# Optimization experiments

Hardware: AMD Instinct MI355X
Metric: run time of the kernel (lower is better)

The kernel has to match this reference:

```python
import math
import jax, jax.numpy as jnp
import numpy as np

N_IMAGES = 32
TOTAL_Q = 2048
TOTAL_KV = 2048
Q_IN = 1024
KV_IN = Q_IN + 9
D_QK = 1024
D_V = 1024
N_HEADS = 16
TEMP = 1.0
SCALER = 1.0 / (TEMP * math.sqrt(D_QK // N_HEADS))


def _ragged_seg_ids(total, n_seg, seed):
    rng = np.random.default_rng(seed)
    lens = rng.multinomial(total - n_seg, np.ones(n_seg) / n_seg) + 1  # every segment nonempty
    return jnp.asarray(np.repeat(np.arange(n_seg), lens), dtype=jnp.int32)


def setup_inputs() -> dict:
    key = jax.random.key(0)
    ks = jax.random.split(key, 12)
    s = 0.02
    return {
        "A": jax.random.normal(ks[0], (TOTAL_Q, Q_IN), jnp.float32),
        "B0": jax.random.normal(ks[1], (TOTAL_KV, KV_IN), jnp.float32),
        "seg_q": _ragged_seg_ids(TOTAL_Q, N_IMAGES, 1),
        "seg_kv": _ragged_seg_ids(TOTAL_KV, N_IMAGES, 2),
        "Wq": jax.random.normal(ks[2], (Q_IN, D_QK), jnp.float32) * s,
        "bq": jax.random.normal(ks[3], (D_QK,), jnp.float32) * s,
        "Wk": jax.random.normal(ks[4], (KV_IN, D_QK), jnp.float32) * s,
        "bk": jax.random.normal(ks[5], (D_QK,), jnp.float32) * s,
        "Wv": jax.random.normal(ks[6], (KV_IN, D_V), jnp.float32) * s,
        "bv": jax.random.normal(ks[7], (D_V,), jnp.float32) * s,
        "Wf": jax.random.normal(ks[8], (D_V, Q_IN), jnp.float32) * s,
        "bf": jax.random.normal(ks[9], (Q_IN,), jnp.float32) * s,
    }


def reference(A, B0, seg_q, seg_kv, Wq, bq, Wk, bk, Wv, bv, Wf, bf):
    # Linear projections on packed rows
    q = (A @ Wq + bq).reshape(TOTAL_Q, N_HEADS, -1)     # [Nq, h, dqk]
    k = (B0 @ Wk + bk).reshape(TOTAL_KV, N_HEADS, -1)   # [Nk, h, dqk]
    v = (B0 @ Wv + bv).reshape(TOTAL_KV, N_HEADS, -1)   # [Nk, h, dv]
    # Per-segment attention expressed as a block mask (same math as the
    # original Python loop over splits)
    scores = jnp.einsum('ihd,khd->ihk', q, k) * SCALER  # [Nq, h, Nk]
    mask = (seg_q[:, None] == seg_kv[None, :])[:, None, :]  # [Nq, 1, Nk]
    neg = jnp.finfo(scores.dtype).min
    w = jax.nn.softmax(jnp.where(mask, scores, neg), axis=-1)
    wv = jnp.einsum('ihk,khd->ihd', w, v).reshape(TOTAL_Q, -1)  # [Nq, h*dv]
    return wv @ Wf + bf  # [Nq, q_in_dim]
```

## Files before the change

### kernel.cpp

```cpp
#include <hip/hip_runtime.h>
#include <hip/hip_bf16.h>
#include <math.h>

#define TOTAL_Q   2048
#define TOTAL_KV  2048
#define QIN       1024
#define KVIN      1033
#define KVIN_P    1056
#define DQK       1024
#define DV        1024
#define KVSTR     2048
#define SCALER    0.125f

typedef __bf16 bf16x8 __attribute__((ext_vector_type(8)));
typedef float  f32x4  __attribute__((ext_vector_type(4)));

__device__ __forceinline__ void glds16(const __hip_bfloat16* g, __bf16* l)
{
    __builtin_amdgcn_global_load_lds(
        (const __attribute__((address_space(1))) void*)g,
        (__attribute__((address_space(3))) void*)l,
        16, 0, 0);
}

__device__ __forceinline__ int stage_cc(int lane)
{
    return (((lane & 3) ^ ((lane >> 3) & 3)) * 8);
}
__device__ __forceinline__ int frag_off(int row, int quad)
{
    return row * 32 + ((quad ^ ((row >> 1) & 3)) * 8);
}

__global__ __launch_bounds__(256)
void prep_k(const float* __restrict__ A,  const float* __restrict__ B0,
            const float* __restrict__ Wq, const float* __restrict__ Wk,
            const float* __restrict__ Wv, const float* __restrict__ Wf,
            __hip_bfloat16* __restrict__ Abf, __hip_bfloat16* __restrict__ B0bf,
            __hip_bfloat16* __restrict__ Wqt, __hip_bfloat16* __restrict__ Wkt,
            __hip_bfloat16* __restrict__ Wvt, __hip_bfloat16* __restrict__ Wft)
{
    const int b   = blockIdx.x;
    const int tid = threadIdx.x;

    if (b < 2048) {
        int i = (b * 256 + tid) * 4;
        float4 f = *(const float4*)(A + i);
        __hip_bfloat16 o[4] = { __float2bfloat16(f.x), __float2bfloat16(f.y),
                                __float2bfloat16(f.z), __float2bfloat16(f.w) };
        *(uint2*)(Abf + i) = *(const uint2*)o;
        return;
    }
    if (b < 4160) {
        int idx = ((b - 2048) * 256 + tid) * 4;
        int r = idx / KVIN_P, c = idx - r * KVIN_P;
        __hip_bfloat16 o[4];
        #pragma unroll
        for (int j = 0; j < 4; ++j)
            o[j] = __float2bfloat16((c + j < KVIN) ? B0[(size_t)r * KVIN + c + j] : 0.f);
        *(uint2*)(B0bf + idx) = *(const uint2*)o;
        return;
    }

    const float* W; __hip_bfloat16* Wt; int K, Kp, k0, n0;
    if (b < 6208) {
        int z = b - 4160;
        W  = (z >= 1024) ? Wf : Wq;
        Wt = (z >= 1024) ? Wft : Wqt;
        K = 1024; Kp = 1024;
        int rem = z & 1023;
        k0 = (rem & 31) * 32; n0 = (rem >> 5) * 32;
    } else {
        int z = b - 6208;
        W  = (z >= 1056) ? Wv : Wk;
        Wt = (z >= 1056) ? Wvt : Wkt;
        K = KVIN; Kp = KVIN_P;
        int rem = (z >= 1056) ? z - 1056 : z;
        k0 = (rem % 33) * 32; n0 = (rem / 33) * 32;
    }
    const int tx = tid & 31, ty = tid >> 5;
    __shared__ float tile[32][33];
    #pragma unroll
    for (int i = 0; i < 4; ++i) {
        int k = k0 + ty + i * 8;
        tile[ty + i * 8][tx] = (k < K) ? W[(size_t)k * 1024 + n0 + tx] : 0.f;
    }
    __syncthreads();
    #pragma unroll
    for (int i = 0; i < 4; ++i) {
        int n = n0 + ty + i * 8;
        Wt[(size_t)n * Kp + k0 + tx] = __float2bfloat16(tile[tx][ty + i * 8]);
    }
}

__global__ __launch_bounds__(256)
void gemm_qkv(const __hip_bfloat16* __restrict__ Abf,
              const __hip_bfloat16* __restrict__ Wqt,
              const float* __restrict__ bq,
              __hip_bfloat16* __restrict__ qb,
              const __hip_bfloat16* __restrict__ B0bf,
              const __hip_bfloat16* __restrict__ Wkvt,
              const float* __restrict__ bk, const float* __restrict__ bv,
              __hip_bfloat16* __restrict__ kvb)
{
    __shared__ __bf16 As[128 * 32];
    __shared__ __bf16 Bs[64 * 32];

    int b = blockIdx.x;
    const __hip_bfloat16 *Ag, *Btg; const float *bias0, *bias1;
    __hip_bfloat16* C; int N, K, bx, by;
    if (b < 256) {
        Ag = Abf; Btg = Wqt; bias0 = bq; bias1 = bq; C = qb;
        N = 1024; K = 1024;
        int xcd = b & 7, i = b >> 3;
        int px = xcd & 3, py = xcd >> 2;
        bx = px * 4 + (i & 3);
        by = py * 8 + (i >> 2);
    } else {
        b -= 256;
        Ag = B0bf; Btg = Wkvt; bias0 = bk; bias1 = bv; C = kvb;
        N = 2048; K = KVIN_P;
        int xcd = b & 7, i = b >> 3;
        int px = xcd & 3, py = xcd >> 2;
        bx = px * 8 + (i & 7);
        by = py * 8 + (i >> 3);
    }
    const int row0 = by * 128, col0 = bx * 64;

    const int tid  = threadIdx.x;
    const int wave = tid >> 6, lane = tid & 63;
    const int quad = lane >> 4, l16 = lane & 15;
    const int wm = (wave >> 1) * 64, wn = (wave & 1) * 32;

    const int cr = lane >> 2;
    const int cc = stage_cc(lane);

    const __hip_bfloat16* gsrc[3];
    __bf16* ldst[3];
    #pragma unroll
    for (int i = 0; i < 3; ++i) {
        int c = wave * 3 + i;
        if (c < 8) {
            gsrc[i] = Ag  + (size_t)(row0 + c * 16 + cr) * K + cc;
            ldst[i] = &As[c * 512];
        } else {
            gsrc[i] = Btg + (size_t)(col0 + (c - 8) * 16 + cr) * K + cc;
            ldst[i] = &Bs[(c - 8) * 512];
        }
    }

    f32x4 acc[4][2] = {};

    for (int k0 = 0; k0 < K; k0 += 32) {
        #pragma unroll
        for (int i = 0; i < 3; ++i)
            glds16(gsrc[i] + k0, ldst[i]);
        __syncthreads();

        bf16x8 af[4], bfr[2];
        #pragma unroll
        for (int mi = 0; mi < 4; ++mi)
            af[mi] = *(const bf16x8*)&As[frag_off(wm + mi * 16 + l16, quad)];
        #pragma unroll
        for (int ni = 0; ni < 2; ++ni)
            bfr[ni] = *(const bf16x8*)&Bs[frag_off(wn + ni * 16 + l16, quad)];

        #pragma unroll
        for (int mi = 0; mi < 4; ++mi)
            #pragma unroll
            for (int ni = 0; ni < 2; ++ni)
                acc[mi][ni] = __builtin_amdgcn_mfma_f32_16x16x32_bf16(
                    af[mi], bfr[ni], acc[mi][ni], 0, 0, 0);
        __syncthreads();
    }

    #pragma unroll
    for (int mi = 0; mi < 4; ++mi) {
        #pragma unroll
        for (int ni = 0; ni < 2; ++ni) {
            const int col = col0 + wn + ni * 16 + l16;
            const float bia = (col < 1024) ? bias0[col] : bias1[col - 1024];
            #pragma unroll
            for (int r = 0; r < 4; ++r) {
                const int row = row0 + wm + mi * 16 + quad * 4 + r;
                C[(size_t)row * N + col] = __float2bfloat16(acc[mi][ni][r] + bia);
            }
        }
    }
}

__global__ __launch_bounds__(256)
void gemm_out(const __hip_bfloat16* __restrict__ A,
              const __hip_bfloat16* __restrict__ Bt,
              const float* __restrict__ bias,
              float* __restrict__ C,
              int M, int N, int K)
{
    __shared__ __bf16 As[128 * 32];
    __shared__ __bf16 Bs[64 * 32];

    int b = blockIdx.x;
    const int xcd = b & 7, i = b >> 3;
    const int px = xcd & 3, py = xcd >> 2;
    const int bx = px * 4 + (i & 3);
    const int by = py * 8 + (i >> 2);

    const int tid  = threadIdx.x;
    const int wave = tid >> 6, lane = tid & 63;
    const int quad = lane >> 4, l16 = lane & 15;
    const int wm = (wave >> 1) * 64;
    const int wn = (wave & 1) * 32;
    const int row0 = by * 128, col0 = bx * 64;

    const int cr = lane >> 2;
    const int cc = stage_cc(lane);

    const __hip_bfloat16* gsrc[3];
    __bf16* ldst[3];
    #pragma unroll
    for (int i2 = 0; i2 < 3; ++i2) {
        int c = wave * 3 + i2;
        if (c < 8) {
            gsrc[i2] = A  + (size_t)(row0 + c * 16 + cr) * K + cc;
            ldst[i2] = &As[c * 512];
        } else {
            gsrc[i2] = Bt + (size_t)(col0 + (c - 8) * 16 + cr) * K + cc;
            ldst[i2] = &Bs[(c - 8) * 512];
        }
    }

    f32x4 acc[4][2] = {};

    for (int k0 = 0; k0 < K; k0 += 32) {
        #pragma unroll
        for (int i2 = 0; i2 < 3; ++i2)
            glds16(gsrc[i2] + k0, ldst[i2]);
        __syncthreads();

        bf16x8 af[4], bfr[2];
        #pragma unroll
        for (int mi = 0; mi < 4; ++mi)
            af[mi] = *(const bf16x8*)&As[frag_off(wm + mi * 16 + l16, quad)];
        #pragma unroll
        for (int ni = 0; ni < 2; ++ni)
            bfr[ni] = *(const bf16x8*)&Bs[frag_off(wn + ni * 16 + l16, quad)];

        #pragma unroll
        for (int mi = 0; mi < 4; ++mi)
            #pragma unroll
            for (int ni = 0; ni < 2; ++ni)
                acc[mi][ni] = __builtin_amdgcn_mfma_f32_16x16x32_bf16(
                    af[mi], bfr[ni], acc[mi][ni], 0, 0, 0);
        __syncthreads();
    }

    #pragma unroll
    for (int mi = 0; mi < 4; ++mi) {
        #pragma unroll
        for (int ni = 0; ni < 2; ++ni) {
            const int col = col0 + wn + ni * 16 + l16;
            const float bia = bias[col];
            #pragma unroll
            for (int r = 0; r < 4; ++r) {
                const int row = row0 + wm + mi * 16 + quad * 4 + r;
                C[(size_t)row * N + col] = acc[mi][ni][r] + bia;
            }
        }
    }
}

#define CH 64

__global__ __launch_bounds__(256)
void attn_mfma(const __hip_bfloat16* __restrict__ qg,
               const __hip_bfloat16* __restrict__ kg,
               const __hip_bfloat16* __restrict__ vg,
               const int* __restrict__ seg_q, const int* __restrict__ seg_kv,
               __hip_bfloat16* __restrict__ wv)
{
    const int h = blockIdx.x & 15;
    const int s = blockIdx.x >> 4;

    __shared__ int sb[4];
    __shared__ __bf16 Ks[CH][72];
    __shared__ __bf16 Vt[64][CH + 8];
    __shared__ __bf16 Ps[4][16][CH + 8];

    if (threadIdx.x == 0) {
        int lo, hi;
        lo = 0; hi = TOTAL_Q;
        while (lo < hi) { int m = (lo + hi) >> 1; if (seg_q[m] <  s) lo = m + 1; else hi = m; }
        sb[0] = lo;
        hi = TOTAL_Q;
        while (lo < hi) { int m = (lo + hi) >> 1; if (seg_q[m] <= s) lo = m + 1; else hi = m; }
        sb[1] = lo;
        lo = 0; hi = TOTAL_KV;
        while (lo < hi) { int m = (lo + hi) >> 1; if (seg_kv[m] <  s) lo = m + 1; else hi = m; }
        sb[2] = lo;
        hi = TOTAL_KV;
        while (lo < hi) { int m = (lo + hi) >> 1; if (seg_kv[m] <= s) lo = m + 1; else hi = m; }
        sb[3] = lo;
    }
    __syncthreads();
    const int qbeg = sb[0], qend = sb[1], kbeg = sb[2], kend = sb[3];

    const int tid  = threadIdx.x;
    const int wave = tid >> 6, lane = tid & 63;
    const int quad = lane >> 4, l16 = lane & 15;

    for (int qt = qbeg; qt < qend; qt += 64) {
        const int qrow = qt + wave * 16 + l16;
        const int qrc  = min(qrow, qend - 1);
        bf16x8 qf[2];
        qf[0] = *(const bf16x8*)(qg + (size_t)qrc * DQK + h * 64 + quad * 8);
        qf[1] = *(const bf16x8*)(qg + (size_t)qrc * DQK + h * 64 + 32 + quad * 8);

        float m[4]  = { -1e30f, -1e30f, -1e30f, -1e30f };
        float l[4]  = { 0.f, 0.f, 0.f, 0.f };
        f32x4 acc[4] = {};

        for (int c0 = kbeg; c0 < kend; c0 += CH) {
            const int cl = min(CH, kend - c0);
            __syncthreads();

            #pragma unroll
            for (int it = 0; it < 2; ++it) {
                int e = (it * 256 + tid) * 8;
                int r = e >> 6, d = e & 63;
                bf16x8 z = {};
                if (r < cl)
                    z = *(const bf16x8*)(kg + (size_t)(c0 + r) * KVSTR + h * 64 + d);
                *(bf16x8*)&Ks[r][d] = z;
            }
            #pragma unroll
            for (int it = 0; it < 4; ++it) {
                int e = (it * 256 + tid) * 4;
                int r = e >> 6, d = e & 63;
                __bf16 t0 = 0, t1 = 0, t2 = 0, t3 = 0;
                if (r < cl) {
                    bf16x8 vv;
                    uint2 uu = *(const uint2*)(vg + (size_t)(c0 + r) * KVSTR + h * 64 + d);
                    *(uint2*)&vv = uu;
                    t0 = vv[0]; t1 = vv[1]; t2 = vv[2]; t3 = vv[3];
                }
                Vt[d + 0][r] = t0; Vt[d + 1][r] = t1;
                Vt[d + 2][r] = t2; Vt[d + 3][r] = t3;
            }
            __syncthreads();

            f32x4 sc[4];
            #pragma unroll
            for (int t = 0; t < 4; ++t) {
                bf16x8 b0 = *(const bf16x8*)&Ks[t * 16 + l16][quad * 8];
                bf16x8 b1 = *(const bf16x8*)&Ks[t * 16 + l16][32 + quad * 8];
                f32x4 z = {};
                z = __builtin_amdgcn_mfma_f32_16x16x32_bf16(qf[0], b0, z, 0, 0, 0);
                z = __builtin_amdgcn_mfma_f32_16x16x32_bf16(qf[1], b1, z, 0, 0, 0);
                sc[t] = z;
            }

            float sv[4][4];
            #pragma unroll
            for (int t = 0; t < 4; ++t) {
                const bool ok = (c0 + t * 16 + l16) < kend;
                #pragma unroll
                for (int r = 0; r < 4; ++r)
                    sv[t][r] = ok ? sc[t][r] * SCALER : -1e30f;
            }

            #pragma unroll
            for (int r = 0; r < 4; ++r) {
                float mx = fmaxf(fmaxf(sv[0][r], sv[1][r]), fmaxf(sv[2][r], sv[3][r]));
                mx = fmaxf(mx, __shfl_xor(mx, 1));
                mx = fmaxf(mx, __shfl_xor(mx, 2));
                mx = fmaxf(mx, __shfl_xor(mx, 4));
                mx = fmaxf(mx, __shfl_xor(mx, 8));
                const float mn = fmaxf(m[r], mx);
                const float alpha = __expf(m[r] - mn);
                m[r] = mn;
                float rs = 0.f;
                #pragma unroll
                for (int t = 0; t < 4; ++t) {
                    const float p = __expf(sv[t][r] - mn);
                    sv[t][r] = p;
                    rs += p;
                }
                rs += __shfl_xor(rs, 1);
                rs += __shfl_xor(rs, 2);
                rs += __shfl_xor(rs, 4);
                rs += __shfl_xor(rs, 8);
                l[r] = l[r] * alpha + rs;
                #pragma unroll
                for (int dt = 0; dt < 4; ++dt) acc[dt][r] *= alpha;
            }

            #pragma unroll
            for (int t = 0; t < 4; ++t)
                #pragma unroll
                for (int r = 0; r < 4; ++r)
                    Ps[wave][quad * 4 + r][t * 16 + l16] = (__bf16)sv[t][r];
            __syncthreads();

            #pragma unroll
            for (int ks = 0; ks < 2; ++ks) {
                bf16x8 pa = *(const bf16x8*)&Ps[wave][l16][ks * 32 + quad * 8];
                #pragma unroll
                for (int dt = 0; dt < 4; ++dt) {
                    bf16x8 vbf = *(const bf16x8*)&Vt[dt * 16 + l16][ks * 32 + quad * 8];
                    acc[dt] = __builtin_amdgcn_mfma_f32_16x16x32_bf16(pa, vbf, acc[dt], 0, 0, 0);
                }
            }
        }

        float inv[4];
        #pragma unroll
        for (int r = 0; r < 4; ++r) inv[r] = 1.f / l[r];
        #pragma unroll
        for (int dt = 0; dt < 4; ++dt) {
            #pragma unroll
            for (int r = 0; r < 4; ++r) {
                const int row = qt + wave * 16 + quad * 4 + r;
                if (row < qend)
                    wv[(size_t)row * DV + h * 64 + dt * 16 + l16] =
                        __float2bfloat16(acc[dt][r] * inv[r]);
            }
        }
    }
}

extern "C" void kernel_launch(void* const* d_in, const int* in_sizes, int n_in,
                              void* d_out, int out_size, void* d_ws, size_t ws_size,
                              hipStream_t stream)
{
    const float* A     = (const float*)d_in[0];
    const float* B0    = (const float*)d_in[1];
    const int*   seg_q = (const int*)  d_in[2];
    const int*   seg_kv= (const int*)  d_in[3];
    const float* Wq    = (const float*)d_in[4];
    const float* bq    = (const float*)d_in[5];
    const float* Wk    = (const float*)d_in[6];
    const float* bk    = (const float*)d_in[7];
    const float* Wv    = (const float*)d_in[8];
    const float* bv    = (const float*)d_in[9];
    const float* Wf    = (const float*)d_in[10];
    const float* bf    = (const float*)d_in[11];
    float* out = (float*)d_out;

    __hip_bfloat16* B0bf = (__hip_bfloat16*)d_ws;
    __hip_bfloat16* Wqt  = B0bf + (size_t)TOTAL_KV * KVIN_P;
    __hip_bfloat16* Wkt  = Wqt  + (size_t)QIN * DQK;
    __hip_bfloat16* Wvt  = Wkt  + (size_t)DQK * KVIN_P;
    __hip_bfloat16* Wft  = Wvt  + (size_t)DV * KVIN_P;
    __hip_bfloat16* Abf  = Wft  + (size_t)DV * QIN;
    __hip_bfloat16* qb   = Abf  + (size_t)TOTAL_Q * QIN;
    __hip_bfloat16* kvb  = qb   + (size_t)TOTAL_Q * DQK;
    __hip_bfloat16* wvb  = Abf;

    const dim3 b256(256);

    prep_k<<<dim3(8320), b256, 0, stream>>>(A, B0, Wq, Wk, Wv, Wf,
                                            Abf, B0bf, Wqt, Wkt, Wvt, Wft);

    gemm_qkv<<<dim3(768), b256, 0, stream>>>(Abf, Wqt, bq, qb,
                                             B0bf, Wkt, bk, bv, kvb);

    attn_mfma<<<dim3(32 * 16), b256, 0, stream>>>(qb, kvb, kvb + 1024, seg_q, seg_kv, wvb);

    gemm_out<<<dim3(256), b256, 0, stream>>>(wvb, Wft, bf, out, TOTAL_Q, QIN, DV);
}
```

Measured before the change: 164.0 us.

## Fuse all four kernels into one persistent kernel with grid barriers

Merges the prep/convert, QKV GEMM, segmented attention and output GEMM kernels into a single persistent kernel of 768 blocks. Stages are separated by software grid-wide barriers built on atomic counters in workspace, which are reset with a memset before each launch. This is meant to remove the launch overhead and tail gaps between kernels. In exchange it depends on all 768 blocks being co-resident (launch bounds set for 3 blocks per CU), and the idle blocks in the attention and output stages add barrier spin cost.

```diff
diff --git a/kernel.cpp b/kernel.cpp
--- a/kernel.cpp
+++ b/kernel.cpp
@@ -11,6 +11,7 @@
 #define DV        1024
 #define KVSTR     2048
 #define SCALER    0.125f
+#define NB        768
 
 typedef __bf16 bf16x8 __attribute__((ext_vector_type(8)));
 typedef float  f32x4  __attribute__((ext_vector_type(4)));
@@ -32,397 +33,391 @@
     return row * 32 + ((quad ^ ((row >> 1) & 3)) * 8);
 }
 
-__global__ __launch_bounds__(256)
-void prep_k(const float* __restrict__ A,  const float* __restrict__ B0,
-            const float* __restrict__ Wq, const float* __restrict__ Wk,
-            const float* __restrict__ Wv, const float* __restrict__ Wf,
-            __hip_bfloat16* __restrict__ Abf, __hip_bfloat16* __restrict__ B0bf,
-            __hip_bfloat16* __restrict__ Wqt, __hip_bfloat16* __restrict__ Wkt,
-            __hip_bfloat16* __restrict__ Wvt, __hip_bfloat16* __restrict__ Wft)
-{
-    const int b   = blockIdx.x;
-    const int tid = threadIdx.x;
-
-    if (b < 2048) {
-        int i = (b * 256 + tid) * 4;
-        float4 f = *(const float4*)(A + i);
-        __hip_bfloat16 o[4] = { __float2bfloat16(f.x), __float2bfloat16(f.y),
-                                __float2bfloat16(f.z), __float2bfloat16(f.w) };
-        *(uint2*)(Abf + i) = *(const uint2*)o;
-        return;
-    }
-    if (b < 4160) {
-        int idx = ((b - 2048) * 256 + tid) * 4;
-        int r = idx / KVIN_P, c = idx - r * KVIN_P;
-        __hip_bfloat16 o[4];
-        #pragma unroll
-        for (int j = 0; j < 4; ++j)
-            o[j] = __float2bfloat16((c + j < KVIN) ? B0[(size_t)r * KVIN + c + j] : 0.f);
-        *(uint2*)(B0bf + idx) = *(const uint2*)o;
-        return;
-    }
-
-    const float* W; __hip_bfloat16* Wt; int K, Kp, k0, n0;
-    if (b < 6208) {
-        int z = b - 4160;
-        W  = (z >= 1024) ? Wf : Wq;
-        Wt = (z >= 1024) ? Wft : Wqt;
-        K = 1024; Kp = 1024;
-        int rem = z & 1023;
-        k0 = (rem & 31) * 32; n0 = (rem >> 5) * 32;
-    } else {
-        int z = b - 6208;
-        W  = (z >= 1056) ? Wv : Wk;
-        Wt = (z >= 1056) ? Wvt : Wkt;
-        K = KVIN; Kp = KVIN_P;
-        int rem = (z >= 1056) ? z - 1056 : z;
-        k0 = (rem % 33) * 32; n0 = (rem / 33) * 32;
-    }
-    const int tx = tid & 31, ty = tid >> 5;
-    __shared__ float tile[32][33];
-    #pragma unroll
-    for (int i = 0; i < 4; ++i) {
-        int k = k0 + ty + i * 8;
-        tile[ty + i * 8][tx] = (k < K) ? W[(size_t)k * 1024 + n0 + tx] : 0.f;
+__device__ __forceinline__ void gbar(int* cnt, int id)
+{
+    __syncthreads();
+    if (threadIdx.x == 0) {
+        __threadfence();
+        __hip_atomic_fetch_add(&cnt[id], 1, __ATOMIC_ACQ_REL, __HIP_MEMORY_SCOPE_AGENT);
+        while (__hip_atomic_load(&cnt[id], __ATOMIC_ACQUIRE, __HIP_MEMORY_SCOPE_AGENT) < NB)
+            __builtin_amdgcn_s_sleep(2);
+        __threadfence();
     }
     __syncthreads();
-    #pragma unroll
-    for (int i = 0; i < 4; ++i) {
-        int n = n0 + ty + i * 8;
-        Wt[(size_t)n * Kp + k0 + tx] = __float2bfloat16(tile[tx][ty + i * 8]);
-    }
-}
-
-__global__ __launch_bounds__(256)
-void gemm_qkv(const __hip_bfloat16* __restrict__ Abf,
-              const __hip_bfloat16* __restrict__ Wqt,
-              const float* __restrict__ bq,
-              __hip_bfloat16* __restrict__ qb,
-              const __hip_bfloat16* __restrict__ B0bf,
-              const __hip_bfloat16* __restrict__ Wkvt,
-              const float* __restrict__ bk, const float* __restrict__ bv,
-              __hip_bfloat16* __restrict__ kvb)
-{
-    __shared__ __bf16 As[128 * 32];
-    __shared__ __bf16 Bs[64 * 32];
-
-    int b = blockIdx.x;
-    const __hip_bfloat16 *Ag, *Btg; const float *bias0, *bias1;
-    __hip_bfloat16* C; int N, K, bx, by;
-    if (b < 256) {
-        Ag = Abf; Btg = Wqt; bias0 = bq; bias1 = bq; C = qb;
-        N = 1024; K = 1024;
-        int xcd = b & 7, i = b >> 3;
-        int px = xcd & 3, py = xcd >> 2;
-        bx = px * 4 + (i & 3);
-        by = py * 8 + (i >> 2);
-    } else {
-        b -= 256;
-        Ag = B0bf; Btg = Wkvt; bias0 = bk; bias1 = bv; C = kvb;
-        N = 2048; K = KVIN_P;
-        int xcd = b & 7, i = b >> 3;
-        int px = xcd & 3, py = xcd >> 2;
-        bx = px * 8 + (i & 7);
-        by = py * 8 + (i >> 3);
-    }
-    const int row0 = by * 128, col0 = bx * 64;
-
-    const int tid  = threadIdx.x;
+}
+
+struct Params {
+    const float *A, *B0;
+    const int   *seg_q, *seg_kv;
+    const float *Wq, *bq, *Wk, *bk, *Wv, *bv, *Wf, *bf;
+    float       *out;
+    __hip_bfloat16 *B0bf, *Wqt, *Wkt, *Wft, *Abf, *qb, *kvb;
+    int *bar;
+};
+
+__global__ __launch_bounds__(256, 3)
+void mega(Params p)
+{
+    __shared__ __align__(16) char smem[27712];
+    const int bid = blockIdx.x;
+    const int tid = threadIdx.x;
     const int wave = tid >> 6, lane = tid & 63;
     const int quad = lane >> 4, l16 = lane & 15;
-    const int wm = (wave >> 1) * 64, wn = (wave & 1) * 32;
-
     const int cr = lane >> 2;
     const int cc = stage_cc(lane);
 
-    const __hip_bfloat16* gsrc[3];
-    __bf16* ldst[3];
-    #pragma unroll
-    for (int i = 0; i < 3; ++i) {
-        int c = wave * 3 + i;
-        if (c < 8) {
-            gsrc[i] = Ag  + (size_t)(row0 + c * 16 + cr) * K + cc;
-            ldst[i] = &As[c * 512];
+    __hip_bfloat16* Wvt = p.Wkt + (size_t)1024 * KVIN_P;
+    __hip_bfloat16* wvb = p.Abf;
+
+    {
+        float (*tile)[33] = (float(*)[33])smem;
+        for (int vb = bid; vb < 8320; vb += NB) {
+            if (vb < 2048) {
+                int i = (vb * 256 + tid) * 4;
+                float4 f = *(const float4*)(p.A + i);
+                __hip_bfloat16 o[4] = { __float2bfloat16(f.x), __float2bfloat16(f.y),
+                                        __float2bfloat16(f.z), __float2bfloat16(f.w) };
+                *(uint2*)(p.Abf + i) = *(const uint2*)o;
+            } else if (vb < 4160) {
+                int idx = ((vb - 2048) * 256 + tid) * 4;
+                int r = idx / KVIN_P, c = idx - r * KVIN_P;
+                __hip_bfloat16 o[4];
+                #pragma unroll
+                for (int j = 0; j < 4; ++j)
+                    o[j] = __float2bfloat16((c + j < KVIN) ? p.B0[(size_t)r * KVIN + c + j] : 0.f);
+                *(uint2*)(p.B0bf + idx) = *(const uint2*)o;
+            } else {
+                const float* W; __hip_bfloat16* Wt; int K, Kp, k0, n0;
+                if (vb < 6208) {
+                    int z = vb - 4160;
+                    W  = (z >= 1024) ? p.Wf : p.Wq;
+                    Wt = (z >= 1024) ? p.Wft : p.Wqt;
+                    K = 1024; Kp = 1024;
+                    int rem = z & 1023;
+                    k0 = (rem & 31) * 32; n0 = (rem >> 5) * 32;
+                } else {
+                    int z = vb - 6208;
+                    W  = (z >= 1056) ? p.Wv : p.Wk;
+                    Wt = (z >= 1056) ? Wvt : p.Wkt;
+                    K = KVIN; Kp = KVIN_P;
+                    int rem = (z >= 1056) ? z - 1056 : z;
+                    k0 = (rem % 33) * 32; n0 = (rem / 33) * 32;
+                }
+                const int tx = tid & 31, ty = tid >> 5;
+                #pragma unroll
+                for (int i = 0; i < 4; ++i) {
+                    int k = k0 + ty + i * 8;
+                    tile[ty + i * 8][tx] = (k < K) ? W[(size_t)k * 1024 + n0 + tx] : 0.f;
+                }
+                __syncthreads();
+                #pragma unroll
+                for (int i = 0; i < 4; ++i) {
+                    int n = n0 + ty + i * 8;
+                    Wt[(size_t)n * Kp + k0 + tx] = __float2bfloat16(tile[tx][ty + i * 8]);
+                }
+                __syncthreads();
+            }
+        }
+    }
+    gbar(p.bar, 0);
+
+    {
+        __bf16* As = (__bf16*)smem;
+        __bf16* Bs = As + 128 * 32;
+
+        int b = bid;
+        const __hip_bfloat16 *Ag, *Btg; const float *bias0, *bias1;
+        __hip_bfloat16* C; int N, K, bx, by;
+        if (b < 256) {
+            Ag = p.Abf; Btg = p.Wqt; bias0 = p.bq; bias1 = p.bq; C = p.qb;
+            N = 1024; K = 1024;
+            int xcd = b & 7, i = b >> 3;
+            int px = xcd & 3, py = xcd >> 2;
+            bx = px * 4 + (i & 3);
+            by = py * 8 + (i >> 2);
         } else {
-            gsrc[i] = Btg + (size_t)(col0 + (c - 8) * 16 + cr) * K + cc;
-            ldst[i] = &Bs[(c - 8) * 512];
+            b -= 256;
+            Ag = p.B0bf; Btg = p.Wkt; bias0 = p.bk; bias1 = p.bv; C = p.kvb;
+            N = 2048; K = KVIN_P;
+            int xcd = b & 7, i = b >> 3;
+            int px = xcd & 3, py = xcd >> 2;
+            bx = px * 8 + (i & 7);
+            by = py * 8 + (i >> 3);
+        }
+        const int row0 = by * 128, col0 = bx * 64;
+        const int wm = (wave >> 1) * 64, wn = (wave & 1) * 32;
+
+        const __hip_bfloat16* gsrc[3];
+        __bf16* ldst[3];
+        #pragma unroll
+        for (int i = 0; i < 3; ++i) {
+            int c = wave * 3 + i;
+            if (c < 8) {
+                gsrc[i] = Ag  + (size_t)(row0 + c * 16 + cr) * K + cc;
+                ldst[i] = &As[c * 512];
+            } else {
+                gsrc[i] = Btg + (size_t)(col0 + (c - 8) * 16 + cr) * K + cc;
+                ldst[i] = &Bs[(c - 8) * 512];
+            }
+        }
+
+        f32x4 acc[4][2] = {};
+
+        for (int k0 = 0; k0 < K; k0 += 32) {
+            #pragma unroll
+            for (int i = 0; i < 3; ++i)
+                glds16(gsrc[i] + k0, ldst[i]);
+            __syncthreads();
+
+            bf16x8 af[4], bfr[2];
+            #pragma unroll
+            for (int mi = 0; mi < 4; ++mi)
+                af[mi] = *(const bf16x8*)&As[frag_off(wm + mi * 16 + l16, quad)];
+            #pragma unroll
+            for (int ni = 0; ni < 2; ++ni)
+                bfr[ni] = *(const bf16x8*)&Bs[frag_off(wn + ni * 16 + l16, quad)];
+
+            #pragma unroll
+            for (int mi = 0; mi < 4; ++mi)
+                #pragma unroll
+                for (int ni = 0; ni < 2; ++ni)
+                    acc[mi][ni] = __builtin_amdgcn_mfma_f32_16x16x32_bf16(
+                        af[mi], bfr[ni], acc[mi][ni], 0, 0, 0);
+            __syncthreads();
+        }
+
+        #pragma unroll
+        for (int mi = 0; mi < 4; ++mi) {
+            #pragma unroll
+            for (int ni = 0; ni < 2; ++ni) {
+                const int col = col0 + wn + ni * 16 + l16;
+                const float bia = (col < 1024) ? bias0[col] : bias1[col - 1024];
+                #pragma unroll
+                for (int r = 0; r < 4; ++r) {
+                    const int row = row0 + wm + mi * 16 + quad * 4 + r;
+                    C[(size_t)row * N + col] = __float2bfloat16(acc[mi][ni][r] + bia);
+                }
+            }
         }
     }
-
-    f32x4 acc[4][2] = {};
-
-    for (int k0 = 0; k0 < K; k0 += 32) {
+    gbar(p.bar, 1);
+
+    if (bid < 512) {
+        __bf16 (*Ks)[72]     = (__bf16(*)[72])smem;
+        __bf16 (*Vt)[72]     = (__bf16(*)[72])(smem + 9216);
+        __bf16 (*Ps)[16][72] = (__bf16(*)[16][72])(smem + 18432);
+        int* sb = (int*)(smem + 27648);
+
+        const int h = bid & 15;
+        const int s = bid >> 4;
+
+        if (tid == 0) {
+            int lo, hi;
+            lo = 0; hi = TOTAL_Q;
+            while (lo < hi) { int m = (lo + hi) >> 1; if (p.seg_q[m] <  s) lo = m + 1; else hi = m; }
+            sb[0] = lo;
+            hi = TOTAL_Q;
+            while (lo < hi) { int m = (lo + hi) >> 1; if (p.seg_q[m] <= s) lo = m + 1; else hi = m; }
+            sb[1] = lo;
+            lo = 0; hi = TOTAL_KV;
+            while (lo < hi) { int m = (lo + hi) >> 1; if (p.seg_kv[m] <  s) lo = m + 1; else hi = m; }
+            sb[2] = lo;
+            hi = TOTAL_KV;
+            while (lo < hi) { int m = (lo + hi) >> 1; if (p.seg_kv[m] <= s) lo = m + 1; else hi = m; }
+            sb[3] = lo;
+        }
+        __syncthreads();
+        const int qbeg = sb[0], qend = sb[1], kbeg = sb[2], kend = sb[3];
+
+        const __hip_bfloat16* kg = p.kvb;
+        const __hip_bfloat16* vg = p.kvb + 1024;
+
+        for (int qt = qbeg; qt < qend; qt += 64) {
+            const int qrow = qt + wave * 16 + l16;
+            const int qrc  = min(qrow, qend - 1);
+            bf16x8 qf[2];
+            qf[0] = *(const bf16x8*)(p.qb + (size_t)qrc * DQK + h * 64 + quad * 8);
+            qf[1] = *(const bf16x8*)(p.qb + (size_t)qrc * DQK + h * 64 + 32 + quad * 8);
+
+            float m[4]  = { -1e30f, -1e30f, -1e30f, -1e30f };
+            float l[4]  = { 0.f, 0.f, 0.f, 0.f };
+            f32x4 acc[4] = {};
+
+            for (int c0 = kbeg; c0 < kend; c0 += 64) {
+                const int cl = min(64, kend - c0);
+                __syncthreads();
+
+                #pragma unroll
+                for (int it = 0; it < 2; ++it) {
+                    int e = (it * 256 + tid) * 8;
+                    int r = e >> 6, d = e & 63;
+                    bf16x8 z = {};
+                    if (r < cl)
+                        z = *(const bf16x8*)(kg + (size_t)(c0 + r) * KVSTR + h * 64 + d);
+                    *(bf16x8*)&Ks[r][d] = z;
+                }
+                #pragma unroll
+                for (int it = 0; it < 4; ++it) {
+                    int e = (it * 256 + tid) * 4;
+                    int r = e >> 6, d = e & 63;
+                    __bf16 t0 = 0, t1 = 0, t2 = 0, t3 = 0;
+                    if (r < cl) {
+                        bf16x8 vv;
+                        uint2 uu = *(const uint2*)(vg + (size_t)(c0 + r) * KVSTR + h * 64 + d);
+                        *(uint2*)&vv = uu;
+                        t0 = vv[0]; t1 = vv[1]; t2 = vv[2]; t3 = vv[3];
+                    }
+                    Vt[d + 0][r] = t0; Vt[d + 1][r] = t1;
+                    Vt[d + 2][r] = t2; Vt[d + 3][r] = t3;
+                }
+                __syncthreads();
+
+                f32x4 sc[4];
+                #pragma unroll
+                for (int t = 0; t < 4; ++t) {
+                    bf16x8 b0 = *(const bf16x8*)&Ks[t * 16 + l16][quad * 8];
+                    bf16x8 b1 = *(const bf16x8*)&Ks[t * 16 + l16][32 + quad * 8];
+                    f32x4 z = {};
+                    z = __builtin_amdgcn_mfma_f32_16x16x32_bf16(qf[0], b0, z, 0, 0, 0);
+                    z = __builtin_amdgcn_mfma_f32_16x16x32_bf16(qf[1], b1, z, 0, 0, 0);
+                    sc[t] = z;
+                }
+
+                float sv[4][4];
+                #pragma unroll
+                for (int t = 0; t < 4; ++t) {
+                    const bool ok = (c0 + t * 16 + l16) < kend;
+                    #pragma unroll
+                    for (int r = 0; r < 4; ++r)
+                        sv[t][r] = ok ? sc[t][r] * SCALER : -1e30f;
+                }
+
+                #pragma unroll
+                for (int r = 0; r < 4; ++r) {
+                    float mx = fmaxf(fmaxf(sv[0][r], sv[1][r]), fmaxf(sv[2][r], sv[3][r]));
+                    mx = fmaxf(mx, __shfl_xor(mx, 1));
+                    mx = fmaxf(mx, __shfl_xor(mx, 2));
+                    mx = fmaxf(mx, __shfl_xor(mx, 4));
+                    mx = fmaxf(mx, __shfl_xor(mx, 8));
+                    const float mn = fmaxf(m[r], mx);
+                    const float alpha = __expf(m[r] - mn);
+                    m[r] = mn;
+                    float rs = 0.f;
+                    #pragma unroll
+                    for (int t = 0; t < 4; ++t) {
+                        const float pw = __expf(sv[t][r] - mn);
+                        sv[t][r] = pw;
+                        rs += pw;
+                    }
+                    rs += __shfl_xor(rs, 1);
+                    rs += __shfl_xor(rs, 2);
+                    rs += __shfl_xor(rs, 4);
+                    rs += __shfl_xor(rs, 8);
+                    l[r] = l[r] * alpha + rs;
+                    #pragma unroll
+                    for (int dt = 0; dt < 4; ++dt) acc[dt][r] *= alpha;
+                }
+
+                #pragma unroll
+                for (int t = 0; t < 4; ++t)
+                    #pragma unroll
+                    for (int r = 0; r < 4; ++r)
+                        Ps[wave][quad * 4 + r][t * 16 + l16] = (__bf16)sv[t][r];
+                __syncthreads();
+
+                #pragma unroll
+                for (int ks = 0; ks < 2; ++ks) {
+                    bf16x8 pa = *(const bf16x8*)&Ps[wave][l16][ks * 32 + quad * 8];
+                    #pragma unroll
+                    for (int dt = 0; dt < 4; ++dt) {
+                        bf16x8 vbf = *(const bf16x8*)&Vt[dt * 16 + l16][ks * 32 + quad * 8];
+                        acc[dt] = __builtin_amdgcn_mfma_f32_16x16x32_bf16(pa, vbf, acc[dt], 0, 0, 0);
+                    }
+                }
+            }
+
+            float inv[4];
+            #pragma unroll
+            for (int r = 0; r < 4; ++r) inv[r] = 1.f / l[r];
+            #pragma unroll
+            for (int dt = 0; dt < 4; ++dt) {
+                #pragma unroll
+                for (int r = 0; r < 4; ++r) {
+                    const int row = qt + wave * 16 + quad * 4 + r;
+                    if (row < qend)
+                        wvb[(size_t)row * DV + h * 64 + dt * 16 + l16] =
+                            __float2bfloat16(acc[dt][r] * inv[r]);
+                }
+            }
+            __syncthreads();
+        }
+    }
+    gbar(p.bar, 2);
+
+    if (bid < 256) {
+        __bf16* As = (__bf16*)smem;
+        __bf16* Bs = As + 128 * 32;
+
+        int b = bid;
+        const int xcd = b & 7, i = b >> 3;
+        const int px = xcd & 3, py = xcd >> 2;
+        const int bx = px * 4 + (i & 3);
+        const int by = py * 8 + (i >> 2);
+
+        const int wm = (wave >> 1) * 64, wn = (wave & 1) * 32;
+        const int row0 = by * 128, col0 = bx * 64;
+        const int K = 1024, N = 1024;
+
+        const __hip_bfloat16* gsrc[3];
+        __bf16* ldst[3];
         #pragma unroll
-        for (int i = 0; i < 3; ++i)
-            glds16(gsrc[i] + k0, ldst[i]);
-        __syncthreads();
-
-        bf16x8 af[4], bfr[2];
+        for (int i2 = 0; i2 < 3; ++i2) {
+            int c = wave * 3 + i2;
+            if (c < 8) {
+                gsrc[i2] = wvb   + (size_t)(row0 + c * 16 + cr) * K + cc;
+                ldst[i2] = &As[c * 512];
+            } else {
+                gsrc[i2] = p.Wft + (size_t)(col0 + (c - 8) * 16 + cr) * K + cc;
+                ldst[i2] = &Bs[(c - 8) * 512];
+            }
+        }
+
+        f32x4 acc[4][2] = {};
+
+        for (int k0 = 0; k0 < K; k0 += 32) {
+            #pragma unroll
+            for (int i2 = 0; i2 < 3; ++i2)
+                glds16(gsrc[i2] + k0, ldst[i2]);
+            __syncthreads();
+
+            bf16x8 af[4], bfr[2];
+            #pragma unroll
+            for (int mi = 0; mi < 4; ++mi)
+                af[mi] = *(const bf16x8*)&As[frag_off(wm + mi * 16 + l16, quad)];
+            #pragma unroll
+            for (int ni = 0; ni < 2; ++ni)
+                bfr[ni] = *(const bf16x8*)&Bs[frag_off(wn + ni * 16 + l16, quad)];
+
+            #pragma unroll
+            for (int mi = 0; mi < 4; ++mi)
+                #pragma unroll
+                for (int ni = 0; ni < 2; ++ni)
+                    acc[mi][ni] = __builtin_amdgcn_mfma_f32_16x16x32_bf16(
+                        af[mi], bfr[ni], acc[mi][ni], 0, 0, 0);
+            __syncthreads();
+        }
+
         #pragma unroll
-        for (int mi = 0; mi < 4; ++mi)
-            af[mi] = *(const bf16x8*)&As[frag_off(wm + mi * 16 + l16, quad)];
-        #pragma unroll
-        for (int ni = 0; ni < 2; ++ni)
-            bfr[ni] = *(const bf16x8*)&Bs[frag_off(wn + ni * 16 + l16, quad)];
-
-        #pragma unroll
-        for (int mi = 0; mi < 4; ++mi)
-            #pragma unroll
-            for (int ni = 0; ni < 2; ++ni)
-                acc[mi][ni] = __builtin_amdgcn_mfma_f32_16x16x32_bf16(
-                    af[mi], bfr[ni], acc[mi][ni], 0, 0, 0);
-        __syncthreads();
-    }
-
-    #pragma unroll
-    for (int mi = 0; mi < 4; ++mi) {
-        #pragma unroll
-        for (int ni = 0; ni < 2; ++ni) {
-            const int col = col0 + wn + ni * 16 + l16;
-            const float bia = (col < 1024) ? bias0[col] : bias1[col - 1024];
-            #pragma unroll
-            for (int r = 0; r < 4; ++r) {
-                const int row = row0 + wm + mi * 16 + quad * 4 + r;
-                C[(size_t)row * N + col] = __float2bfloat16(acc[mi][ni][r] + bia);
-            }
-        }
-    }
-}
-
-__global__ __launch_bounds__(256)
-void gemm_out(const __hip_bfloat16* __restrict__ A,
-              const __hip_bfloat16* __restrict__ Bt,
-              const float* __restrict__ bias,
-              float* __restrict__ C,
-              int M, int N, int K)
-{
-    __shared__ __bf16 As[128 * 32];
-    __shared__ __bf16 Bs[64 * 32];
-
-    int b = blockIdx.x;
-    const int xcd = b & 7, i = b >> 3;
-    const int px = xcd & 3, py = xcd >> 2;
-    const int bx = px * 4 + (i & 3);
-    const int by = py * 8 + (i >> 2);
-
-    const int tid  = threadIdx.x;
-    const int wave = tid >> 6, lane = tid & 63;
-    const int quad = lane >> 4, l16 = lane & 15;
-    const int wm = (wave >> 1) * 64;
-    const int wn = (wave & 1) * 32;
-    const int row0 = by * 128, col0 = bx * 64;
-
-    const int cr = lane >> 2;
-    const int cc = stage_cc(lane);
-
-    const __hip_bfloat16* gsrc[3];
-    __bf16* ldst[3];
-    #pragma unroll
-    for (int i2 = 0; i2 < 3; ++i2) {
-        int c = wave * 3 + i2;
-        if (c < 8) {
-            gsrc[i2] = A  + (size_t)(row0 + c * 16 + cr) * K + cc;
-            ldst[i2] = &As[c * 512];
-        } else {
-            gsrc[i2] = Bt + (size_t)(col0 + (c - 8) * 16 + cr) * K + cc;
-            ldst[i2] = &Bs[(c - 8) * 512];
-        }
-    }
-
-    f32x4 acc[4][2] = {};
-
-    for (int k0 = 0; k0 < K; k0 += 32) {
-        #pragma unroll
-        for (int i2 = 0; i2 < 3; ++i2)
-            glds16(gsrc[i2] + k0, ldst[i2]);
-        __syncthreads();
-
-        bf16x8 af[4], bfr[2];
-        #pragma unroll
-        for (int mi = 0; mi < 4; ++mi)
-            af[mi] = *(const bf16x8*)&As[frag_off(wm + mi * 16 + l16, quad)];
-        #pragma unroll
-        for (int ni = 0; ni < 2; ++ni)
-            bfr[ni] = *(const bf16x8*)&Bs[frag_off(wn + ni * 16 + l16, quad)];
-
-        #pragma unroll
-        for (int mi = 0; mi < 4; ++mi)
-            #pragma unroll
-            for (int ni = 0; ni < 2; ++ni)
-                acc[mi][ni] = __builtin_amdgcn_mfma_f32_16x16x32_bf16(
-                    af[mi], bfr[ni], acc[mi][ni], 0, 0, 0);
-        __syncthreads();
-    }
-
-    #pragma unroll
-    for (int mi = 0; mi < 4; ++mi) {
-        #pragma unroll
-        for (int ni = 0; ni < 2; ++ni) {
-            const int col = col0 + wn + ni * 16 + l16;
-            const float bia = bias[col];
-            #pragma unroll
-            for (int r = 0; r < 4; ++r) {
-                const int row = row0 + wm + mi * 16 + quad * 4 + r;
-                C[(size_t)row * N + col] = acc[mi][ni][r] + bia;
-            }
-        }
-    }
-}
-
-#define CH 64
-
-__global__ __launch_bounds__(256)
-void attn_mfma(const __hip_bfloat16* __restrict__ qg,
-               const __hip_bfloat16* __restrict__ kg,
-               const __hip_bfloat16* __restrict__ vg,
-               const int* __restrict__ seg_q, const int* __restrict__ seg_kv,
-               __hip_bfloat16* __restrict__ wv)
-{
-    const int h = blockIdx.x & 15;
-    const int s = blockIdx.x >> 4;
-
-    __shared__ int sb[4];
-    __shared__ __bf16 Ks[CH][72];
-    __shared__ __bf16 Vt[64][CH + 8];
-    __shared__ __bf16 Ps[4][16][CH + 8];
-
-    if (threadIdx.x == 0) {
-        int lo, hi;
-        lo = 0; hi = TOTAL_Q;
-        while (lo < hi) { int m = (lo + hi) >> 1; if (seg_q[m] <  s) lo = m + 1; else hi = m; }
-        sb[0] = lo;
-        hi = TOTAL_Q;
-        while (lo < hi) { int m = (lo + hi) >> 1; if (seg_q[m] <= s) lo = m + 1; else hi = m; }
-        sb[1] = lo;
-        lo = 0; hi = TOTAL_KV;
-        while (lo < hi) { int m = (lo + hi) >> 1; if (seg_kv[m] <  s) lo = m + 1; else hi = m; }
-        sb[2] = lo;
-        hi = TOTAL_KV;
-        while (lo < hi) { int m = (lo + hi) >> 1; if (seg_kv[m] <= s) lo = m + 1; else hi = m; }
-        sb[3] = lo;
-    }
-    __syncthreads();
-    const int qbeg = sb[0], qend = sb[1], kbeg = sb[2], kend = sb[3];
-
-    const int tid  = threadIdx.x;
-    const int wave = tid >> 6, lane = tid & 63;
-    const int quad = lane >> 4, l16 = lane & 15;
-
-    for (int qt = qbeg; qt < qend; qt += 64) {
-        const int qrow = qt + wave * 16 + l16;
-        const int qrc  = min(qrow, qend - 1);
-        bf16x8 qf[2];
-        qf[0] = *(const bf16x8*)(qg + (size_t)qrc * DQK + h * 64 + quad * 8);
-        qf[1] = *(const bf16x8*)(qg + (size_t)qrc * DQK + h * 64 + 32 + quad * 8);
-
-        float m[4]  = { -1e30f, -1e30f, -1e30f, -1e30f };
-        float l[4]  = { 0.f, 0.f, 0.f, 0.f };
-        f32x4 acc[4] = {};
-
-        for (int c0 = kbeg; c0 < kend; c0 += CH) {
-            const int cl = min(CH, kend - c0);
-            __syncthreads();
-
-            #pragma unroll
-            for (int it = 0; it < 2; ++it) {
-                int e = (it * 256 + tid) * 8;
-                int r = e >> 6, d = e & 63;
-                bf16x8 z = {};
-                if (r < cl)
-                    z = *(const bf16x8*)(kg + (size_t)(c0 + r) * KVSTR + h * 64 + d);
-                *(bf16x8*)&Ks[r][d] = z;
-            }
-            #pragma unroll
-            for (int it = 0; it < 4; ++it) {
-                int e = (it * 256 + tid) * 4;
-                int r = e >> 6, d = e & 63;
-                __bf16 t0 = 0, t1 = 0, t2 = 0, t3 = 0;
-                if (r < cl) {
-                    bf16x8 vv;
-                    uint2 uu = *(const uint2*)(vg + (size_t)(c0 + r) * KVSTR + h * 64 + d);
-                    *(uint2*)&vv = uu;
-                    t0 = vv[0]; t1 = vv[1]; t2 = vv[2]; t3 = vv[3];
-                }
-                Vt[d + 0][r] = t0; Vt[d + 1][r] = t1;
-                Vt[d + 2][r] = t2; Vt[d + 3][r] = t3;
-            }
-            __syncthreads();
-
-            f32x4 sc[4];
-            #pragma unroll
-            for (int t = 0; t < 4; ++t) {
-                bf16x8 b0 = *(const bf16x8*)&Ks[t * 16 + l16][quad * 8];
-                bf16x8 b1 = *(const bf16x8*)&Ks[t * 16 + l16][32 + quad * 8];
-                f32x4 z = {};
-                z = __builtin_amdgcn_mfma_f32_16x16x32_bf16(qf[0], b0, z, 0, 0, 0);
-                z = __builtin_amdgcn_mfma_f32_16x16x32_bf16(qf[1], b1, z, 0, 0, 0);
-                sc[t] = z;
-            }
-
-            float sv[4][4];
-            #pragma unroll
-            for (int t = 0; t < 4; ++t) {
-                const bool ok = (c0 + t * 16 + l16) < kend;
-                #pragma unroll
-                for (int r = 0; r < 4; ++r)
-                    sv[t][r] = ok ? sc[t][r] * SCALER : -1e30f;
-            }
-
-            #pragma unroll
-            for (int r = 0; r < 4; ++r) {
-                float mx = fmaxf(fmaxf(sv[0][r], sv[1][r]), fmaxf(sv[2][r], sv[3][r]));
-                mx = fmaxf(mx, __shfl_xor(mx, 1));
-                mx = fmaxf(mx, __shfl_xor(mx, 2));
-                mx = fmaxf(mx, __shfl_xor(mx, 4));
-                mx = fmaxf(mx, __shfl_xor(mx, 8));
-                const float mn = fmaxf(m[r], mx);
-                const float alpha = __expf(m[r] - mn);
-                m[r] = mn;
-                float rs = 0.f;
-                #pragma unroll
-                for (int t = 0; t < 4; ++t) {
-                    const float p = __expf(sv[t][r] - mn);
-                    sv[t][r] = p;
-                    rs += p;
-                }
-                rs += __shfl_xor(rs, 1);
-                rs += __shfl_xor(rs, 2);
-                rs += __shfl_xor(rs, 4);
-                rs += __shfl_xor(rs, 8);
-                l[r] = l[r] * alpha + rs;
-                #pragma unroll
-                for (int dt = 0; dt < 4; ++dt) acc[dt][r] *= alpha;
-            }
-
-            #pragma unroll
-            for (int t = 0; t < 4; ++t)
-                #pragma unroll
-                for (int r = 0; r < 4; ++r)
-                    Ps[wave][quad * 4 + r][t * 16 + l16] = (__bf16)sv[t][r];
-            __syncthreads();
-
-            #pragma unroll
-            for (int ks = 0; ks < 2; ++ks) {
-                bf16x8 pa = *(const bf16x8*)&Ps[wave][l16][ks * 32 + quad * 8];
-                #pragma unroll
-                for (int dt = 0; dt < 4; ++dt) {
-                    bf16x8 vbf = *(const bf16x8*)&Vt[dt * 16 + l16][ks * 32 + quad * 8];
-                    acc[dt] = __builtin_amdgcn_mfma_f32_16x16x32_bf16(pa, vbf, acc[dt], 0, 0, 0);
-                }
-            }
-        }
-
-        float inv[4];
-        #pragma unroll
-        for (int r = 0; r < 4; ++r) inv[r] = 1.f / l[r];
-        #pragma unroll
-        for (int dt = 0; dt < 4; ++dt) {
-            #pragma unroll
-            for (int r = 0; r < 4; ++r) {
-                const int row = qt + wave * 16 + quad * 4 + r;
-                if (row < qend)
-                    wv[(size_t)row * DV + h * 64 + dt * 16 + l16] =
-                        __float2bfloat16(acc[dt][r] * inv[r]);
+        for (int mi = 0; mi < 4; ++mi) {
+            #pragma unroll
+            for (int ni = 0; ni < 2; ++ni) {
+                const int col = col0 + wn + ni * 16 + l16;
+                const float bia = p.bf[col];
+                #pragma unroll
+                for (int r = 0; r < 4; ++r) {
+                    const int row = row0 + wm + mi * 16 + quad * 4 + r;
+                    p.out[(size_t)row * N + col] = acc[mi][ni][r] + bia;
+                }
             }
         }
     }
@@ -432,39 +427,30 @@
                               void* d_out, int out_size, void* d_ws, size_t ws_size,
                               hipStream_t stream)
 {
-    const float* A     = (const float*)d_in[0];
-    const float* B0    = (const float*)d_in[1];
-    const int*   seg_q = (const int*)  d_in[2];
-    const int*   seg_kv= (const int*)  d_in[3];
-    const float* Wq    = (const float*)d_in[4];
-    const float* bq    = (const float*)d_in[5];
-    const float* Wk    = (const float*)d_in[6];
-    const float* bk    = (const float*)d_in[7];
-    const float* Wv    = (const float*)d_in[8];
-    const float* bv    = (const float*)d_in[9];
-    const float* Wf    = (const float*)d_in[10];
-    const float* bf    = (const float*)d_in[11];
-    float* out = (float*)d_out;
-
-    __hip_bfloat16* B0bf = (__hip_bfloat16*)d_ws;
-    __hip_bfloat16* Wqt  = B0bf + (size_t)TOTAL_KV * KVIN_P;
-    __hip_bfloat16* Wkt  = Wqt  + (size_t)QIN * DQK;
-    __hip_bfloat16* Wvt  = Wkt  + (size_t)DQK * KVIN_P;
-    __hip_bfloat16* Wft  = Wvt  + (size_t)DV * KVIN_P;
-    __hip_bfloat16* Abf  = Wft  + (size_t)DV * QIN;
-    __hip_bfloat16* qb   = Abf  + (size_t)TOTAL_Q * QIN;
-    __hip_bfloat16* kvb  = qb   + (size_t)TOTAL_Q * DQK;
-    __hip_bfloat16* wvb  = Abf;
-
-    const dim3 b256(256);
-
-    prep_k<<<dim3(8320), b256, 0, stream>>>(A, B0, Wq, Wk, Wv, Wf,
-                                            Abf, B0bf, Wqt, Wkt, Wvt, Wft);
-
-    gemm_qkv<<<dim3(768), b256, 0, stream>>>(Abf, Wqt, bq, qb,
-                                             B0bf, Wkt, bk, bv, kvb);
-
-    attn_mfma<<<dim3(32 * 16), b256, 0, stream>>>(qb, kvb, kvb + 1024, seg_q, seg_kv, wvb);
-
-    gemm_out<<<dim3(256), b256, 0, stream>>>(wvb, Wft, bf, out, TOTAL_Q, QIN, DV);
-}
+    Params p;
+    p.A      = (const float*)d_in[0];
+    p.B0     = (const float*)d_in[1];
+    p.seg_q  = (const int*)  d_in[2];
+    p.seg_kv = (const int*)  d_in[3];
+    p.Wq     = (const float*)d_in[4];
+    p.bq     = (const float*)d_in[5];
+    p.Wk     = (const float*)d_in[6];
+    p.bk     = (const float*)d_in[7];
+    p.Wv     = (const float*)d_in[8];
+    p.bv     = (const float*)d_in[9];
+    p.Wf     = (const float*)d_in[10];
+    p.bf     = (const float*)d_in[11];
+    p.out    = (float*)d_out;
+
+    p.B0bf = (__hip_bfloat16*)d_ws;
+    p.Wqt  = p.B0bf + (size_t)TOTAL_KV * KVIN_P;
+    p.Wkt  = p.Wqt  + (size_t)QIN * DQK;
+    p.Wft  = p.Wkt  + (size_t)2 * DQK * KVIN_P;
+    p.Abf  = p.Wft  + (size_t)DV * QIN;
+    p.qb   = p.Abf  + (size_t)TOTAL_Q * QIN;
+    p.kvb  = p.qb   + (size_t)TOTAL_Q * DQK;
+    p.bar  = (int*)((char*)d_ws + ((size_t)64 << 20));
+
+    hipMemsetAsync(p.bar, 0, 16, stream);
+    mega<<<dim3(NB), dim3(256), 0, stream>>>(p);
+}
```

Measured after the change: 564.2 us. 244% more time.
